# Performance work log

Measured on AMD Instinct MI355X. Metric: run time of the kernel, lower is better.

The kernel has to match this reference:

```python
import jax, jax.numpy as jnp
import numpy as np

DIM = 256
HEADS = 8
DIM_HEAD = 64
INNER = HEADS * DIM_HEAD  # 512
B, N = 4, 1024


def setup_inputs() -> dict:
    key = jax.random.key(0)
    ks = jax.random.split(key, 7)
    x = jax.random.normal(ks[0], (B, N, DIM), dtype=jnp.float32)
    attn_bias = jax.random.normal(ks[1], (B, HEADS, N, N), dtype=jnp.float32)
    s = 1.0 / np.sqrt(DIM)
    Wq = jax.random.normal(ks[2], (DIM, INNER), dtype=jnp.float32) * s
    Wkv = jax.random.normal(ks[3], (DIM, 2 * INNER), dtype=jnp.float32) * s
    # to_out initialized to zero in the torch module; use small random so output is non-trivial
    Wo = jax.random.normal(ks[4], (INNER, DIM), dtype=jnp.float32) * (1.0 / np.sqrt(INNER))
    bo = jnp.zeros((DIM,), dtype=jnp.float32)
    # gating initialized weight=0, bias=1 -> sigmoid(1); use small random weight + bias 1
    Wg = jax.random.normal(ks[5], (DIM, INNER), dtype=jnp.float32) * 0.02
    bg = jnp.ones((INNER,), dtype=jnp.float32)
    return {"x": x, "attn_bias": attn_bias, "Wq": Wq, "Wkv": Wkv,
            "Wo": Wo, "bo": bo, "Wg": Wg, "bg": bg}


def reference(x, attn_bias, Wq, Wkv, Wo, bo, Wg, bg):
    b, n, _ = x.shape
    scale = DIM_HEAD ** -0.5
    q = x @ Wq                                    # [b, n, inner]
    kv = x @ Wkv                                  # [b, n, 2*inner]
    k, v = jnp.split(kv, 2, axis=-1)
    def split_heads(t):
        return t.reshape(b, n, HEADS, DIM_HEAD).transpose(0, 2, 1, 3)  # [b,h,n,d]
    q, k, v = split_heads(q) * scale, split_heads(k), split_heads(v)
    dots = jnp.einsum('bhid,bhjd->bhij', q, k) + attn_bias
    # explicit max-subtract then softmax (matches original; numerically identical)
    attn = jax.nn.softmax(dots, axis=-1)
    out = jnp.einsum('bhij,bhjd->bhid', attn, v)  # [b,h,n,d]
    out = out.transpose(0, 2, 1, 3).reshape(b, n, INNER)
    gates = jax.nn.sigmoid(x @ Wg + bg)
    out = out * gates
    return out @ Wo + bo
```

## Files before the change

kernel.cpp:

```cpp
#include <hip/hip_runtime.h>

typedef unsigned short u16;
typedef unsigned int u32;
typedef __attribute__((ext_vector_type(8))) __bf16 bf16x8;
typedef __attribute__((ext_vector_type(4))) float floatx4;

#define DEV __device__ __forceinline__

DEV u16 f2bf(float f) {
  u32 u = __builtin_bit_cast(u32, f);
  u = (u + 0x7fffu + ((u >> 16) & 1u)) >> 16;
  return (u16)u;
}
DEV float bf2f(u16 h) {
  u32 u = ((u32)h) << 16;
  return __builtin_bit_cast(float, u);
}
DEV floatx4 MFMA(bf16x8 a, bf16x8 b, floatx4 c) {
  return __builtin_amdgcn_mfma_f32_16x16x32_bf16(a, b, c, 0, 0, 0);
}

__global__ void convert_k(const float* __restrict__ x, const float* __restrict__ Wq,
                          const float* __restrict__ Wkv, const float* __restrict__ Wg,
                          const float* __restrict__ Wo,
                          u16* __restrict__ xb, u16* __restrict__ WcatT, u16* __restrict__ WoT) {
  int i = blockIdx.x * 256 + threadIdx.x;
  if (i < 1048576) { xb[i] = f2bf(x[i]); return; }
  i -= 1048576;
  if (i < 524288) {
    int n = i >> 8, kk = i & 255;
    float v;
    if (n < 512) v = Wq[kk * 512 + n];
    else if (n < 1536) v = Wkv[kk * 1024 + (n - 512)];
    else v = Wg[kk * 512 + (n - 1536)];
    WcatT[i] = f2bf(v);
    return;
  }
  i -= 524288;
  if (i < 131072) {
    int n = i >> 9, kk = i & 511;
    WoT[i] = f2bf(Wo[kk * 256 + n]);
  }
}

__global__ __launch_bounds__(256, 4) void gemm_qkvg(
    const u16* __restrict__ xb, const u16* __restrict__ WcatT, const float* __restrict__ bg,
    u16* __restrict__ qb, u16* __restrict__ kb, u16* __restrict__ vT, u16* __restrict__ gb) {
  __shared__ __attribute__((aligned(16))) u16 As[128 * 40];
  __shared__ __attribute__((aligned(16))) u16 Bs[64 * 40];
  __shared__ __attribute__((aligned(16))) u16 Lt[64 * 132];
  const int tid = threadIdx.x;
  const int wave = tid >> 6, lane = tid & 63;
  const int lane15 = lane & 15, quad = lane >> 4;
  const int rm0 = blockIdx.x * 128;
  const int cn0 = blockIdx.y * 64;
  const int wm = (wave & 1) * 64, wn = (wave >> 1) * 32;
  const int rowA = tid >> 1, segA = (tid & 1) * 16;
  const int rowB = tid >> 2, segB = (tid & 3) * 8;
  floatx4 acc[4][2] = {};
  uint4 a0 = *(const uint4*)(xb + (rm0 + rowA) * 256 + segA);
  uint4 a1 = *(const uint4*)(xb + (rm0 + rowA) * 256 + segA + 8);
  uint4 b0 = *(const uint4*)(WcatT + (cn0 + rowB) * 256 + segB);
#pragma unroll 1
  for (int k0 = 0; k0 < 256; k0 += 32) {
    __syncthreads();
    *(uint4*)(As + rowA * 40 + segA) = a0;
    *(uint4*)(As + rowA * 40 + segA + 8) = a1;
    *(uint4*)(Bs + rowB * 40 + segB) = b0;
    __syncthreads();
    if (k0 < 224) {
      a0 = *(const uint4*)(xb + (rm0 + rowA) * 256 + k0 + 32 + segA);
      a1 = *(const uint4*)(xb + (rm0 + rowA) * 256 + k0 + 32 + segA + 8);
      b0 = *(const uint4*)(WcatT + (cn0 + rowB) * 256 + k0 + 32 + segB);
    }
    bf16x8 af[4], bfr[2];
#pragma unroll
    for (int mt = 0; mt < 4; ++mt) af[mt] = *(const bf16x8*)(As + (wm + mt * 16 + lane15) * 40 + quad * 8);
#pragma unroll
    for (int nt = 0; nt < 2; ++nt) bfr[nt] = *(const bf16x8*)(Bs + (wn + nt * 16 + lane15) * 40 + quad * 8);
#pragma unroll
    for (int mt = 0; mt < 4; ++mt)
#pragma unroll
      for (int nt = 0; nt < 2; ++nt)
        acc[mt][nt] = MFMA(af[mt], bfr[nt], acc[mt][nt]);
  }
  const bool is_v = (cn0 >= 1024) && (cn0 < 1536);
#pragma unroll
  for (int mt = 0; mt < 4; ++mt)
#pragma unroll
    for (int nt = 0; nt < 2; ++nt)
#pragma unroll
      for (int r = 0; r < 4; ++r) {
        int row = rm0 + wm + mt * 16 + quad * 4 + r;
        int col = cn0 + wn + nt * 16 + lane15;
        float v = acc[mt][nt][r];
        int b = row >> 10, n = row & 1023;
        if (col < 512) {
          int h = col >> 6, d = col & 63;
          qb[((b * 8 + h) * 1024 + n) * 64 + d] = f2bf(v * 0.125f);
        } else if (col < 1024) {
          int c = col - 512, h = c >> 6, d = c & 63;
          kb[((b * 8 + h) * 1024 + n) * 64 + d] = f2bf(v);
        } else if (col < 1536) {
          int d = (col - 1024) & 63;
          Lt[d * 132 + (wm + mt * 16 + quad * 4 + r)] = f2bf(v);
        } else {
          int c = col - 1536;
          float g = 1.0f / (1.0f + __expf(-(v + bg[c])));
          gb[row * 512 + c] = f2bf(g);
        }
      }
  if (is_v) {
    __syncthreads();
    int d = tid >> 2, seg = (tid & 3) * 32;
    int b = rm0 >> 10, n_base = rm0 & 1023;
    int h = (cn0 - 1024) >> 6;
    u16* dst = vT + ((size_t)((b * 8 + h) * 64 + d)) * 1024 + n_base + seg;
    const u16* src = Lt + d * 132 + seg;
#pragma unroll
    for (int u = 0; u < 4; ++u)
      *(uint4*)(dst + u * 8) = *(const uint4*)(src + u * 8);
  }
}

__global__ __launch_bounds__(256, 3) void attn_part_k(
    const u16* __restrict__ qb, const u16* __restrict__ kb, const u16* __restrict__ vT,
    const float* __restrict__ bias,
    float* __restrict__ po, float* __restrict__ pl) {
  __shared__ __attribute__((aligned(16))) u16 Ps[4 * 16 * 72];
  const int tid = threadIdx.x;
  const int wave = tid >> 6, lane = tid & 63;
  const int lane15 = lane & 15, quad = lane >> 4;
  const int bh = blockIdx.x;
  const int q0 = blockIdx.y * 64;
  const int kc = blockIdx.z;

  bf16x8 qf0, qf1;
  {
    const u16* qrow = qb + ((size_t)(bh * 1024 + q0 + wave * 16 + lane15)) * 64 + quad * 8;
    qf0 = *(const bf16x8*)(qrow);
    qf1 = *(const bf16x8*)(qrow + 32);
  }
  bf16x8 ones;
#pragma unroll
  for (int e = 0; e < 8; ++e) ones[e] = __builtin_bit_cast(__bf16, (u16)0x3F80);

  floatx4 oacc[4] = {};
  floatx4 lacc = {};

  u16* Pw = Ps + wave * (16 * 72);
  const u16* kp = kb + (size_t)bh * 65536;
  const u16* vp = vT + (size_t)bh * 65536;
  const float* bb = bias + ((size_t)(bh * 1024 + q0 + wave * 16 + quad * 4)) * 1024;

  bf16x8 nK0[4], nK1[4];
  float nBV[4][4];
  {
    const int kb0 = kc * 512;
#pragma unroll
    for (int j = 0; j < 4; ++j) {
      const u16* kr = kp + ((size_t)(kb0 + j * 16 + lane15)) * 64 + quad * 8;
      nK0[j] = *(const bf16x8*)kr;
      nK1[j] = *(const bf16x8*)(kr + 32);
    }
#pragma unroll
    for (int j = 0; j < 4; ++j)
#pragma unroll
      for (int r = 0; r < 4; ++r)
        nBV[j][r] = bb[(size_t)r * 1024 + kb0 + j * 16 + lane15];
  }

#pragma unroll
  for (int kt = 0; kt < 8; ++kt) {
    const int kb0 = kc * 512 + kt * 64;
    bf16x8 cK0[4], cK1[4];
    float cBV[4][4];
#pragma unroll
    for (int j = 0; j < 4; ++j) { cK0[j] = nK0[j]; cK1[j] = nK1[j]; }
#pragma unroll
    for (int j = 0; j < 4; ++j)
#pragma unroll
      for (int r = 0; r < 4; ++r) cBV[j][r] = nBV[j][r];

    floatx4 s[4];
#pragma unroll
    for (int j = 0; j < 4; ++j) {
      floatx4 z = {};
      z = MFMA(qf0, cK0[j], z);
      s[j] = MFMA(qf1, cK1[j], z);
    }
    bf16x8 vf0[4];
#pragma unroll
    for (int dt = 0; dt < 4; ++dt)
      vf0[dt] = *(const bf16x8*)(vp + ((size_t)(dt * 16 + lane15)) * 1024 + kb0 + quad * 8);
    if (kt < 7) {
      const int kn = kb0 + 64;
#pragma unroll
      for (int j = 0; j < 4; ++j) {
        const u16* kr = kp + ((size_t)(kn + j * 16 + lane15)) * 64 + quad * 8;
        nK0[j] = *(const bf16x8*)kr;
        nK1[j] = *(const bf16x8*)(kr + 32);
      }
#pragma unroll
      for (int j = 0; j < 4; ++j)
#pragma unroll
        for (int r = 0; r < 4; ++r)
          nBV[j][r] = bb[(size_t)r * 1024 + kn + j * 16 + lane15];
    }
#pragma unroll
    for (int j = 0; j < 4; ++j)
#pragma unroll
      for (int r = 0; r < 4; ++r)
        s[j][r] = __expf(s[j][r] + cBV[j][r] - 8.0f);
    bf16x8 vf1[4];
#pragma unroll
    for (int dt = 0; dt < 4; ++dt)
      vf1[dt] = *(const bf16x8*)(vp + ((size_t)(dt * 16 + lane15)) * 1024 + kb0 + 32 + quad * 8);
#pragma unroll
    for (int j = 0; j < 4; ++j)
#pragma unroll
      for (int r = 0; r < 4; ++r)
        Pw[(quad * 4 + r) * 72 + j * 16 + lane15] = f2bf(s[j][r]);
    bf16x8 pf0 = *(const bf16x8*)(Pw + lane15 * 72 + quad * 8);
    bf16x8 pf1 = *(const bf16x8*)(Pw + lane15 * 72 + 32 + quad * 8);

    lacc = MFMA(pf0, ones, lacc);
    lacc = MFMA(pf1, ones, lacc);
#pragma unroll
    for (int dt = 0; dt < 4; ++dt) {
      oacc[dt] = MFMA(pf0, vf0[dt], oacc[dt]);
      oacc[dt] = MFMA(pf1, vf1[dt], oacc[dt]);
    }
  }

  float* poW = po + ((size_t)(kc * 32 + bh)) * 65536;
#pragma unroll
  for (int dt = 0; dt < 4; ++dt)
#pragma unroll
    for (int r = 0; r < 4; ++r) {
      int qrow = q0 + wave * 16 + quad * 4 + r;
      poW[(size_t)qrow * 64 + dt * 16 + lane15] = oacc[dt][r];
    }
  if (lane15 == 0) {
#pragma unroll
    for (int r = 0; r < 4; ++r) {
      int qrow = q0 + wave * 16 + quad * 4 + r;
      pl[kc * 32768 + bh * 1024 + qrow] = lacc[r];
    }
  }
}

__global__ __launch_bounds__(256) void attn_merge_k(
    const float* __restrict__ po, const float* __restrict__ pl,
    const u16* __restrict__ gb, u16* __restrict__ ogb) {
  int t = blockIdx.x * 256 + threadIdx.x;
  int row = t >> 4;
  int dseg = (t & 15) * 4;
  float inv = 1.0f / (pl[row] + pl[32768 + row]);
  float4 o0 = *(const float4*)(po + (size_t)row * 64 + dseg);
  float4 o1 = *(const float4*)(po + ((size_t)(32768 + row)) * 64 + dseg);
  int bh = row >> 10, q = row & 1023;
  int h = bh & 7, b = bh >> 3;
  size_t gi = ((size_t)(b * 1024 + q)) * 512 + h * 64 + dseg;
  u16 g4[4];
  *(uint2*)g4 = *(const uint2*)(gb + gi);
  u16 r4[4];
  r4[0] = f2bf((o0.x + o1.x) * inv * bf2f(g4[0]));
  r4[1] = f2bf((o0.y + o1.y) * inv * bf2f(g4[1]));
  r4[2] = f2bf((o0.z + o1.z) * inv * bf2f(g4[2]));
  r4[3] = f2bf((o0.w + o1.w) * inv * bf2f(g4[3]));
  *(uint2*)(ogb + gi) = *(uint2*)r4;
}

__global__ __launch_bounds__(256, 4) void gemm_out_part(
    const u16* __restrict__ og, const u16* __restrict__ WoT, float* __restrict__ pout) {
  __shared__ __attribute__((aligned(16))) u16 As[128 * 40];
  __shared__ __attribute__((aligned(16))) u16 Bs[64 * 40];
  const int tid = threadIdx.x;
  const int wave = tid >> 6, lane = tid & 63;
  const int lane15 = lane & 15, quad = lane >> 4;
  const int rm0 = blockIdx.x * 128;
  const int cn0 = blockIdx.y * 64;
  const int kc = blockIdx.z;
  const int wm = (wave & 1) * 64, wn = (wave >> 1) * 32;
  const int rowA = tid >> 1, segA = (tid & 1) * 16;
  const int rowB = tid >> 2, segB = (tid & 3) * 8;
  floatx4 acc[4][2] = {};
  uint4 a0 = *(const uint4*)(og + (rm0 + rowA) * 512 + kc * 128 + segA);
  uint4 a1 = *(const uint4*)(og + (rm0 + rowA) * 512 + kc * 128 + segA + 8);
  uint4 b0 = *(const uint4*)(WoT + (cn0 + rowB) * 512 + kc * 128 + segB);
#pragma unroll 1
  for (int s = 0; s < 4; ++s) {
    const int k0 = kc * 128 + s * 32;
    __syncthreads();
    *(uint4*)(As + rowA * 40 + segA) = a0;
    *(uint4*)(As + rowA * 40 + segA + 8) = a1;
    *(uint4*)(Bs + rowB * 40 + segB) = b0;
    __syncthreads();
    if (s < 3) {
      a0 = *(const uint4*)(og + (rm0 + rowA) * 512 + k0 + 32 + segA);
      a1 = *(const uint4*)(og + (rm0 + rowA) * 512 + k0 + 32 + segA + 8);
      b0 = *(const uint4*)(WoT + (cn0 + rowB) * 512 + k0 + 32 + segB);
    }
    bf16x8 af[4], bfr[2];
#pragma unroll
    for (int mt = 0; mt < 4; ++mt) af[mt] = *(const bf16x8*)(As + (wm + mt * 16 + lane15) * 40 + quad * 8);
#pragma unroll
    for (int nt = 0; nt < 2; ++nt) bfr[nt] = *(const bf16x8*)(Bs + (wn + nt * 16 + lane15) * 40 + quad * 8);
#pragma unroll
    for (int mt = 0; mt < 4; ++mt)
#pragma unroll
      for (int nt = 0; nt < 2; ++nt)
        acc[mt][nt] = MFMA(af[mt], bfr[nt], acc[mt][nt]);
  }
  float* pw = pout + (size_t)kc * 1048576;
#pragma unroll
  for (int mt = 0; mt < 4; ++mt)
#pragma unroll
    for (int nt = 0; nt < 2; ++nt)
#pragma unroll
      for (int r = 0; r < 4; ++r) {
        int row = rm0 + wm + mt * 16 + quad * 4 + r;
        int col = cn0 + wn + nt * 16 + lane15;
        pw[(size_t)row * 256 + col] = acc[mt][nt][r];
      }
}

__global__ __launch_bounds__(256) void reduce4_bo(
    const float* __restrict__ pout, const float* __restrict__ bo, float* __restrict__ out) {
  int g = blockIdx.x * 256 + threadIdx.x;
  const float4* p = (const float4*)pout;
  float4 s0 = p[g], s1 = p[g + 262144], s2 = p[g + 524288], s3 = p[g + 786432];
  int col = (g * 4) & 255;
  float4 bb = *(const float4*)(bo + col);
  float4 r;
  r.x = s0.x + s1.x + s2.x + s3.x + bb.x;
  r.y = s0.y + s1.y + s2.y + s3.y + bb.y;
  r.z = s0.z + s1.z + s2.z + s3.z + bb.z;
  r.w = s0.w + s1.w + s2.w + s3.w + bb.w;
  ((float4*)out)[g] = r;
}

extern "C" void kernel_launch(void* const* d_in, const int* in_sizes, int n_in,
                              void* d_out, int out_size, void* d_ws, size_t ws_size,
                              hipStream_t stream) {
  const float* x = (const float*)d_in[0];
  const float* bias = (const float*)d_in[1];
  const float* Wq = (const float*)d_in[2];
  const float* Wkv = (const float*)d_in[3];
  const float* Wo = (const float*)d_in[4];
  const float* bo = (const float*)d_in[5];
  const float* Wg = (const float*)d_in[6];
  const float* bg = (const float*)d_in[7];
  float* out = (float*)d_out;
  char* ws = (char*)d_ws;
  u16* xb    = (u16*)(ws);
  u16* WcatT = (u16*)(ws + 2097152);
  u16* WoT   = (u16*)(ws + 3145728);
  u16* qb    = (u16*)(ws + 3407872);
  u16* kb    = (u16*)(ws + 7602176);
  u16* vTb   = (u16*)(ws + 11796480);
  u16* gb    = (u16*)(ws + 15990784);
  u16* ogb   = (u16*)(ws + 20185088);
  float* po  = (float*)(ws + 24379392);
  float* pl  = (float*)(ws);
  float* pout = po;

  convert_k<<<6656, 256, 0, stream>>>(x, Wq, Wkv, Wg, Wo, xb, WcatT, WoT);
  dim3 g1(32, 32);
  gemm_qkvg<<<g1, 256, 0, stream>>>(xb, WcatT, bg, qb, kb, vTb, gb);
  dim3 g2(32, 16, 2);
  attn_part_k<<<g2, 256, 0, stream>>>(qb, kb, vTb, bias, po, pl);
  attn_merge_k<<<2048, 256, 0, stream>>>(po, pl, gb, ogb);
  dim3 g3(32, 4, 4);
  gemm_out_part<<<g3, 256, 0, stream>>>(ogb, WoT, pout);
  reduce4_bo<<<1024, 256, 0, stream>>>(pout, bo, out);
}
```

Before: 287.8 us.

## Store K/V in MFMA-fragment layout and stage tiles via direct global-to-LDS loads

```diff
diff --git a/kernel.cpp b/kernel.cpp
--- a/kernel.cpp
+++ b/kernel.cpp
@@ -4,6 +4,8 @@
 typedef unsigned int u32;
 typedef __attribute__((ext_vector_type(8))) __bf16 bf16x8;
 typedef __attribute__((ext_vector_type(4))) float floatx4;
+typedef const __attribute__((address_space(1))) unsigned char glob_u8;
+typedef __attribute__((address_space(3))) unsigned char lds_u8;
 
 #define DEV __device__ __forceinline__
 
@@ -45,10 +47,9 @@
 
 __global__ __launch_bounds__(256, 4) void gemm_qkvg(
     const u16* __restrict__ xb, const u16* __restrict__ WcatT, const float* __restrict__ bg,
-    u16* __restrict__ qb, u16* __restrict__ kb, u16* __restrict__ vT, u16* __restrict__ gb) {
+    u16* __restrict__ qb, u16* __restrict__ kfrag, u16* __restrict__ vfrag, u16* __restrict__ gb) {
   __shared__ __attribute__((aligned(16))) u16 As[128 * 40];
   __shared__ __attribute__((aligned(16))) u16 Bs[64 * 40];
-  __shared__ __attribute__((aligned(16))) u16 Lt[64 * 132];
   const int tid = threadIdx.x;
   const int wave = tid >> 6, lane = tid & 63;
   const int lane15 = lane & 15, quad = lane >> 4;
@@ -84,7 +85,6 @@
       for (int nt = 0; nt < 2; ++nt)
         acc[mt][nt] = MFMA(af[mt], bfr[nt], acc[mt][nt]);
   }
-  const bool is_v = (cn0 >= 1024) && (cn0 < 1536);
 #pragma unroll
   for (int mt = 0; mt < 4; ++mt)
 #pragma unroll
@@ -100,33 +100,31 @@
           qb[((b * 8 + h) * 1024 + n) * 64 + d] = f2bf(v * 0.125f);
         } else if (col < 1024) {
           int c = col - 512, h = c >> 6, d = c & 63;
-          kb[((b * 8 + h) * 1024 + n) * 64 + d] = f2bf(v);
+          int bh2 = b * 8 + h;
+          int t = n >> 4, l15 = n & 15;
+          int half = d >> 5, qd = (d >> 3) & 3, e = d & 7;
+          kfrag[(size_t)bh2 * 65536 + t * 1024 + half * 512 + (qd * 16 + l15) * 8 + e] = f2bf(v);
         } else if (col < 1536) {
-          int d = (col - 1024) & 63;
-          Lt[d * 132 + (wm + mt * 16 + quad * 4 + r)] = f2bf(v);
+          int c = col - 1024, h = c >> 6, d = c & 63;
+          int bh2 = b * 8 + h;
+          int t64 = n >> 6, ck = (n >> 5) & 1, qd = (n >> 3) & 3, e = n & 7;
+          int dt = d >> 4, l15 = d & 15;
+          vfrag[(size_t)bh2 * 65536 + t64 * 4096 + dt * 1024 + ck * 512 + (qd * 16 + l15) * 8 + e] = f2bf(v);
         } else {
           int c = col - 1536;
           float g = 1.0f / (1.0f + __expf(-(v + bg[c])));
           gb[row * 512 + c] = f2bf(g);
         }
       }
-  if (is_v) {
-    __syncthreads();
-    int d = tid >> 2, seg = (tid & 3) * 32;
-    int b = rm0 >> 10, n_base = rm0 & 1023;
-    int h = (cn0 - 1024) >> 6;
-    u16* dst = vT + ((size_t)((b * 8 + h) * 64 + d)) * 1024 + n_base + seg;
-    const u16* src = Lt + d * 132 + seg;
-#pragma unroll
-    for (int u = 0; u < 4; ++u)
-      *(uint4*)(dst + u * 8) = *(const uint4*)(src + u * 8);
-  }
 }
 
 __global__ __launch_bounds__(256, 3) void attn_part_k(
-    const u16* __restrict__ qb, const u16* __restrict__ kb, const u16* __restrict__ vT,
+    const u16* __restrict__ qb, const u16* __restrict__ kfrag, const u16* __restrict__ vfrag,
     const float* __restrict__ bias,
     float* __restrict__ po, float* __restrict__ pl) {
+  __shared__ __attribute__((aligned(16))) u16 Kt[4096];
+  __shared__ __attribute__((aligned(16))) u16 Vt[4096];
+  __shared__ __attribute__((aligned(16))) float Bt[4096];
   __shared__ __attribute__((aligned(16))) u16 Ps[4 * 16 * 72];
   const int tid = threadIdx.x;
   const int wave = tid >> 6, lane = tid & 63;
@@ -149,73 +147,44 @@
   floatx4 lacc = {};
 
   u16* Pw = Ps + wave * (16 * 72);
-  const u16* kp = kb + (size_t)bh * 65536;
-  const u16* vp = vT + (size_t)bh * 65536;
-  const float* bb = bias + ((size_t)(bh * 1024 + q0 + wave * 16 + quad * 4)) * 1024;
-
-  bf16x8 nK0[4], nK1[4];
-  float nBV[4][4];
-  {
-    const int kb0 = kc * 512;
-#pragma unroll
-    for (int j = 0; j < 4; ++j) {
-      const u16* kr = kp + ((size_t)(kb0 + j * 16 + lane15)) * 64 + quad * 8;
-      nK0[j] = *(const bf16x8*)kr;
-      nK1[j] = *(const bf16x8*)(kr + 32);
-    }
-#pragma unroll
-    for (int j = 0; j < 4; ++j)
-#pragma unroll
-      for (int r = 0; r < 4; ++r)
-        nBV[j][r] = bb[(size_t)r * 1024 + kb0 + j * 16 + lane15];
-  }
-
-#pragma unroll
+  const u16* kp = kfrag + (size_t)bh * 65536;
+  const u16* vp = vfrag + (size_t)bh * 65536;
+
+#pragma unroll 1
   for (int kt = 0; kt < 8; ++kt) {
     const int kb0 = kc * 512 + kt * 64;
-    bf16x8 cK0[4], cK1[4];
-    float cBV[4][4];
-#pragma unroll
-    for (int j = 0; j < 4; ++j) { cK0[j] = nK0[j]; cK1[j] = nK1[j]; }
+    const u16* kS = kp + kb0 * 64;
+    const u16* vS = vp + kb0 * 64;
+#pragma unroll
+    for (int c = 0; c < 2; ++c) {
+      int ch = wave * 2 + c;
+      __builtin_amdgcn_global_load_lds((glob_u8*)(kS + ch * 512 + lane * 8),
+                                       (lds_u8*)(Kt + ch * 512), 16, 0, 0);
+      __builtin_amdgcn_global_load_lds((glob_u8*)(vS + ch * 512 + lane * 8),
+                                       (lds_u8*)(Vt + ch * 512), 16, 0, 0);
+    }
+#pragma unroll
+    for (int c = 0; c < 4; ++c) {
+      int ch = wave * 4 + c;
+      const float* bS = bias + ((size_t)(bh * 1024 + q0 + ch * 4 + (lane >> 4))) * 1024 + kb0 + (lane & 15) * 4;
+      __builtin_amdgcn_global_load_lds((glob_u8*)bS, (lds_u8*)(Bt + ch * 256), 16, 0, 0);
+    }
+    __syncthreads();
+
+    floatx4 s[4];
+#pragma unroll
+    for (int j = 0; j < 4; ++j) {
+      bf16x8 kf0 = *(const bf16x8*)(Kt + j * 1024 + lane * 8);
+      bf16x8 kf1 = *(const bf16x8*)(Kt + j * 1024 + 512 + lane * 8);
+      floatx4 z = {};
+      z = MFMA(qf0, kf0, z);
+      s[j] = MFMA(qf1, kf1, z);
+    }
 #pragma unroll
     for (int j = 0; j < 4; ++j)
 #pragma unroll
-      for (int r = 0; r < 4; ++r) cBV[j][r] = nBV[j][r];
-
-    floatx4 s[4];
-#pragma unroll
-    for (int j = 0; j < 4; ++j) {
-      floatx4 z = {};
-      z = MFMA(qf0, cK0[j], z);
-      s[j] = MFMA(qf1, cK1[j], z);
-    }
-    bf16x8 vf0[4];
-#pragma unroll
-    for (int dt = 0; dt < 4; ++dt)
-      vf0[dt] = *(const bf16x8*)(vp + ((size_t)(dt * 16 + lane15)) * 1024 + kb0 + quad * 8);
-    if (kt < 7) {
-      const int kn = kb0 + 64;
-#pragma unroll
-      for (int j = 0; j < 4; ++j) {
-        const u16* kr = kp + ((size_t)(kn + j * 16 + lane15)) * 64 + quad * 8;
-        nK0[j] = *(const bf16x8*)kr;
-        nK1[j] = *(const bf16x8*)(kr + 32);
-      }
-#pragma unroll
-      for (int j = 0; j < 4; ++j)
-#pragma unroll
-        for (int r = 0; r < 4; ++r)
-          nBV[j][r] = bb[(size_t)r * 1024 + kn + j * 16 + lane15];
-    }
-#pragma unroll
-    for (int j = 0; j < 4; ++j)
-#pragma unroll
       for (int r = 0; r < 4; ++r)
-        s[j][r] = __expf(s[j][r] + cBV[j][r] - 8.0f);
-    bf16x8 vf1[4];
-#pragma unroll
-    for (int dt = 0; dt < 4; ++dt)
-      vf1[dt] = *(const bf16x8*)(vp + ((size_t)(dt * 16 + lane15)) * 1024 + kb0 + 32 + quad * 8);
+        s[j][r] = __expf(s[j][r] + Bt[(wave * 16 + quad * 4 + r) * 64 + j * 16 + lane15] - 8.0f);
 #pragma unroll
     for (int j = 0; j < 4; ++j)
 #pragma unroll
@@ -228,9 +197,12 @@
     lacc = MFMA(pf1, ones, lacc);
 #pragma unroll
     for (int dt = 0; dt < 4; ++dt) {
-      oacc[dt] = MFMA(pf0, vf0[dt], oacc[dt]);
-      oacc[dt] = MFMA(pf1, vf1[dt], oacc[dt]);
-    }
+      bf16x8 vf0 = *(const bf16x8*)(Vt + dt * 1024 + lane * 8);
+      bf16x8 vf1 = *(const bf16x8*)(Vt + dt * 1024 + 512 + lane * 8);
+      oacc[dt] = MFMA(pf0, vf0, oacc[dt]);
+      oacc[dt] = MFMA(pf1, vf1, oacc[dt]);
+    }
+    __syncthreads();
   }
 
   float* poW = po + ((size_t)(kc * 32 + bh)) * 65536;
@@ -358,8 +330,8 @@
   u16* WcatT = (u16*)(ws + 2097152);
   u16* WoT   = (u16*)(ws + 3145728);
   u16* qb    = (u16*)(ws + 3407872);
-  u16* kb    = (u16*)(ws + 7602176);
-  u16* vTb   = (u16*)(ws + 11796480);
+  u16* kfrag = (u16*)(ws + 7602176);
+  u16* vfrag = (u16*)(ws + 11796480);
   u16* gb    = (u16*)(ws + 15990784);
   u16* ogb   = (u16*)(ws + 20185088);
   float* po  = (float*)(ws + 24379392);
@@ -368,9 +340,9 @@
 
   convert_k<<<6656, 256, 0, stream>>>(x, Wq, Wkv, Wg, Wo, xb, WcatT, WoT);
   dim3 g1(32, 32);
-  gemm_qkvg<<<g1, 256, 0, stream>>>(xb, WcatT, bg, qb, kb, vTb, gb);
+  gemm_qkvg<<<g1, 256, 0, stream>>>(xb, WcatT, bg, qb, kfrag, vfrag, gb);
   dim3 g2(32, 16, 2);
-  attn_part_k<<<g2, 256, 0, stream>>>(qb, kb, vTb, bias, po, pl);
+  attn_part_k<<<g2, 256, 0, stream>>>(qb, kfrag, vfrag, bias, po, pl);
   attn_merge_k<<<2048, 256, 0, stream>>>(po, pl, gb, ogb);
   dim3 g3(32, 4, 4);
   gemm_out_part<<<g3, 256, 0, stream>>>(ogb, WoT, pout);
```

New measurement: 263.6 us. 8.4% less time.
